# Optimization experiments

Hardware: AMD Instinct MI355X
Metric: run time of the kernel (lower is better)

The kernel has to match this reference:

```python
import jax, jax.numpy as jnp
import numpy as np

SEQ, BATCH, HIDDEN = 4096, 16, 512

def setup_inputs() -> dict:
    key = jax.random.key(0)
    kf, kx, kh = jax.random.split(key, 3)
    f = jax.random.uniform(kf, (SEQ, BATCH, HIDDEN), dtype=jnp.float32)
    x = jax.random.normal(kx, (SEQ, BATCH, HIDDEN), dtype=jnp.float32)
    hidden_init = jax.random.normal(kh, (BATCH, HIDDEN), dtype=jnp.float32)
    return {"f": f, "x": x, "hidden_init": hidden_init}

def reference(f, x, hidden_init):
    # h_t = f_t * x_t + (1 - f_t) * h_{t-1}
    # Linear recurrence h_t = a_t * h_{t-1} + b_t with a = 1-f, b = f*x.
    # Solved with an associative scan: compose (a1,b1) then (a2,b2) ->
    # (a1*a2, a2*b1 + b2). After the scan, A_t = prod(a_1..a_t) and
    # B_t = h_t assuming h_0 = 0, so h_t = B_t + A_t * h_init.
    a = 1.0 - f                      # (S, B, H)
    b = f * x                        # (S, B, H)

    def combine(c1, c2):
        a1, b1 = c1
        a2, b2 = c2
        return (a1 * a2, a2 * b1 + b2)

    A, B = jax.lax.associative_scan(combine, (a, b), axis=0)
    return B + A * hidden_init[None, :, :]
```

## Files before the change

kernel.cpp:

```cpp
#include <hip/hip_runtime.h>


#define SQ      4096
#define NC4     2048
#define NCH     8192
#define TT      32
#define NCHUNK  (SQ / TT)
#define NBLK    256
#define SEGS    16
#define CPS     (NCHUNK / SEGS)

#define AGGA_OFF  0u
#define AGGB_OFF  4194304u
#define SEGA_OFF  8388608u
#define SEGB_OFF  8912896u
#define SEGH_OFF  9437184u
#define BAR_OFF   9961472u
#define WS_NEED   (BAR_OFF + 2048u)

typedef float floatx4 __attribute__((ext_vector_type(4)));

#define FM_B(B,F,X) \
  B.x = fmaf(F.x, X.x - B.x, B.x); B.y = fmaf(F.y, X.y - B.y, B.y); \
  B.z = fmaf(F.z, X.z - B.z, B.z); B.w = fmaf(F.w, X.w - B.w, B.w);
#define FM_A(A,F) \
  A.x = fmaf(-F.x, A.x, A.x); A.y = fmaf(-F.y, A.y, A.y); \
  A.z = fmaf(-F.z, A.z, A.z); A.w = fmaf(-F.w, A.w, A.w);

__device__ __forceinline__ void grid_barrier(unsigned* bar, int gen)
{
  __syncthreads();
  if (threadIdx.x == 0) {
    __threadfence();
    __hip_atomic_fetch_add(&bar[(gen * 8 + (blockIdx.x & 7)) * 16], 1u,
                           __ATOMIC_RELEASE, __HIP_MEMORY_SCOPE_AGENT);
    unsigned sum;
    do {
      sum = 0;
#pragma unroll
      for (int s = 0; s < 8; ++s)
        sum += __hip_atomic_load(&bar[(gen * 8 + s) * 16],
                                 __ATOMIC_RELAXED, __HIP_MEMORY_SCOPE_AGENT);
      if (sum < (unsigned)NBLK) __builtin_amdgcn_s_sleep(8);
    } while (sum < (unsigned)NBLK);
    __threadfence();
  }
  __syncthreads();
}

__global__ __launch_bounds__(512, 2)
void fm_fused(const floatx4* __restrict__ f4, const floatx4* __restrict__ x4,
              const float* __restrict__ h0, char* __restrict__ ws,
              floatx4* __restrict__ out4)
{
  floatx4*  aggA4 = (floatx4*)(ws + AGGA_OFF);
  floatx4*  aggB4 = (floatx4*)(ws + AGGB_OFF);
  float*    aggAs = (float*)(ws + AGGA_OFF);
  float*    aggBs = (float*)(ws + AGGB_OFF);
  float*    segA  = (float*)(ws + SEGA_OFF);
  float*    segB  = (float*)(ws + SEGB_OFF);
  float*    segH  = (float*)(ws + SEGH_OFF);
  unsigned* bar   = (unsigned*)(ws + BAR_OFF);

  const int bid = blockIdx.x, tid = threadIdx.x;
  const int chunk = bid >> 1;
  const int c0 = ((bid & 1) << 10) + tid;
  const int c1 = c0 + 512;
  const size_t tbase = (size_t)chunk * TT * NC4;

  {
    floatx4 A0 = {1.f,1.f,1.f,1.f}, A1 = {1.f,1.f,1.f,1.f};
    floatx4 B0 = {0.f,0.f,0.f,0.f}, B1 = {0.f,0.f,0.f,0.f};
#pragma unroll 8
    for (int t = 0; t < TT; ++t) {
      const size_t r = tbase + (size_t)t * NC4;
      const floatx4 F0 = f4[r + c0], X0 = x4[r + c0];
      const floatx4 F1 = f4[r + c1], X1 = x4[r + c1];
      FM_B(B0, F0, X0)  FM_A(A0, F0)
      FM_B(B1, F1, X1)  FM_A(A1, F1)
    }
    aggA4[(size_t)chunk * NC4 + c0] = A0;
    aggA4[(size_t)chunk * NC4 + c1] = A1;
    aggB4[(size_t)chunk * NC4 + c0] = B0;
    aggB4[(size_t)chunk * NC4 + c1] = B1;
  }
  grid_barrier(bar, 0);

  {
    const int g = bid * 512 + tid;
    const int chain = g & (NCH - 1);
    const int seg   = g >> 13;
    float a = 1.f, b = 0.f;
#pragma unroll
    for (int i = 0; i < CPS; ++i) {
      const size_t idx = (size_t)(seg * CPS + i) * NCH + chain;
      const float ac = aggAs[idx], bc = aggBs[idx];
      b = fmaf(ac, b, bc);
      a *= ac;
    }
    segA[seg * NCH + chain] = a;
    segB[seg * NCH + chain] = b;
  }
  grid_barrier(bar, 1);

  if (bid < 16) {
    const int chain = bid * 512 + tid;
    float h = h0[chain];
#pragma unroll
    for (int s = 0; s < SEGS; ++s) {
      segH[s * NCH + chain] = h;
      h = fmaf(segA[s * NCH + chain], h, segB[s * NCH + chain]);
    }
  }
  grid_barrier(bar, 2);

  {
    const int g = bid * 512 + tid;
    const int chain = g & (NCH - 1);
    const int seg   = g >> 13;
    float h = segH[seg * NCH + chain];
    float a[CPS], b[CPS];
#pragma unroll
    for (int i = 0; i < CPS; ++i) {
      const size_t idx = (size_t)(seg * CPS + i) * NCH + chain;
      a[i] = aggAs[idx];
      b[i] = aggBs[idx];
    }
#pragma unroll
    for (int i = 0; i < CPS; ++i) {
      const size_t idx = (size_t)(seg * CPS + i) * NCH + chain;
      aggBs[idx] = h;
      h = fmaf(a[i], h, b[i]);
    }
  }
  grid_barrier(bar, 3);

  {
    floatx4 H0 = aggB4[(size_t)chunk * NC4 + c0];
    floatx4 H1 = aggB4[(size_t)chunk * NC4 + c1];
#pragma unroll 8
    for (int t = 0; t < TT; ++t) {
      const size_t r = tbase + (size_t)t * NC4;
      const floatx4 F0 = f4[r + c0], X0 = x4[r + c0];
      const floatx4 F1 = f4[r + c1], X1 = x4[r + c1];
      FM_B(H0, F0, X0)
      FM_B(H1, F1, X1)
      __builtin_nontemporal_store(H0, &out4[r + c0]);
      __builtin_nontemporal_store(H1, &out4[r + c1]);
    }
  }
}

#define FTT     16
#define FNCHUNK (SQ / FTT)

__global__ __launch_bounds__(256, 4)
void fm_agg(const floatx4* __restrict__ f4, const floatx4* __restrict__ x4,
            floatx4* __restrict__ aggA, floatx4* __restrict__ aggB)
{
  const int tid   = threadIdx.x;
  const int chunk = blockIdx.x >> 3;
  const int col   = ((blockIdx.x & 7) << 8) + tid;
  const size_t base = (size_t)(chunk * FTT) * NC4 + col;

  floatx4 A = {1.f,1.f,1.f,1.f}, B = {0.f,0.f,0.f,0.f};
#pragma unroll 8
  for (int t = 0; t < FTT; ++t) {
    const floatx4 F = f4[base + (size_t)t * NC4];
    const floatx4 X = x4[base + (size_t)t * NC4];
    FM_B(B, F, X)  FM_A(A, F)
  }
  aggA[(size_t)chunk * NC4 + col] = A;
  aggB[(size_t)chunk * NC4 + col] = B;
}

__global__ __launch_bounds__(256, 4)
void fm_mid(const float* __restrict__ A, float* __restrict__ B,
            const float* __restrict__ h0)
{
  const int chain = blockIdx.x * 256 + threadIdx.x;
  float h = h0[chain];
  for (int cb = 0; cb < FNCHUNK / 16; ++cb) {
    float a[16], b[16];
#pragma unroll
    for (int i = 0; i < 16; ++i) {
      const size_t idx = (size_t)(cb * 16 + i) * NCH + chain;
      a[i] = A[idx];
      b[i] = B[idx];
    }
#pragma unroll
    for (int i = 0; i < 16; ++i) {
      const size_t idx = (size_t)(cb * 16 + i) * NCH + chain;
      B[idx] = h;
      h = fmaf(a[i], h, b[i]);
    }
  }
}

__global__ __launch_bounds__(256, 4)
void fm_apply(const floatx4* __restrict__ f4, const floatx4* __restrict__ x4,
              const floatx4* __restrict__ hprev4, floatx4* __restrict__ out4)
{
  const int tid   = threadIdx.x;
  const int chunk = (FNCHUNK - 1) - (blockIdx.x >> 3);
  const int col   = ((blockIdx.x & 7) << 8) + tid;
  const size_t base = (size_t)(chunk * FTT) * NC4 + col;

  floatx4 h = hprev4[(size_t)chunk * NC4 + col];
#pragma unroll 8
  for (int t = 0; t < FTT; ++t) {
    const floatx4 F = f4[base + (size_t)t * NC4];
    const floatx4 X = x4[base + (size_t)t * NC4];
    FM_B(h, F, X)
    __builtin_nontemporal_store(h, &out4[base + (size_t)t * NC4]);
  }
}

__global__ void fm_naive(const floatx4* __restrict__ f4, const floatx4* __restrict__ x4,
                         const floatx4* __restrict__ h04, floatx4* __restrict__ out4)
{
  const int col = blockIdx.x * blockDim.x + threadIdx.x;
  if (col >= NC4) return;
  floatx4 h = h04[col];
  for (int t = 0; t < SQ; ++t) {
    const size_t idx = (size_t)t * NC4 + col;
    const floatx4 F = f4[idx], X = x4[idx];
    FM_B(h, F, X)
    out4[idx] = h;
  }
}

extern "C" void kernel_launch(void* const* d_in, const int* in_sizes, int n_in,
                              void* d_out, int out_size, void* d_ws, size_t ws_size,
                              hipStream_t stream)
{
  const floatx4* f4  = (const floatx4*)d_in[0];
  const floatx4* x4  = (const floatx4*)d_in[1];
  const float*   h0  = (const float*)d_in[2];
  floatx4* out4 = (floatx4*)d_out;

  static int coopOK = -1;
  if (coopOK < 0) {
    int dev = 0;
    hipGetDevice(&dev);
    hipDeviceProp_t prop;
    int blocksPerCU = 0;
    if (hipGetDeviceProperties(&prop, dev) == hipSuccess &&
        prop.cooperativeLaunch &&
        hipOccupancyMaxActiveBlocksPerMultiprocessor(
            &blocksPerCU, (const void*)fm_fused, 512, 0) == hipSuccess &&
        blocksPerCU >= 1 &&
        (long long)blocksPerCU * prop.multiProcessorCount >= NBLK) {
      coopOK = 1;
    } else {
      coopOK = 0;
    }
  }

  if (ws_size >= WS_NEED && coopOK == 1) {
    char* ws = (char*)d_ws;
    hipMemsetAsync(ws + BAR_OFF, 0, 2048, stream);
    void* args[5];
    args[0] = (void*)&f4; args[1] = (void*)&x4; args[2] = (void*)&h0;
    args[3] = (void*)&ws; args[4] = (void*)&out4;
    hipError_t e = hipLaunchCooperativeKernel((const void*)fm_fused,
                                              dim3(NBLK), dim3(512),
                                              args, 0, stream);
    if (e == hipSuccess) return;
    coopOK = 0;
  }

  const size_t AGG = (size_t)FNCHUNK * NC4 * 16;
  if (ws_size >= 2 * AGG) {
    floatx4* aggA = (floatx4*)d_ws;
    floatx4* aggB = (floatx4*)((char*)d_ws + AGG);
    fm_agg<<<FNCHUNK * 8, 256, 0, stream>>>(f4, x4, aggA, aggB);
    fm_mid<<<NCH / 256, 256, 0, stream>>>((const float*)aggA,
                                          (float*)aggB, h0);
    fm_apply<<<FNCHUNK * 8, 256, 0, stream>>>(f4, x4, (const floatx4*)aggB, out4);
  } else {
    fm_naive<<<(NC4 + 255) / 256, 256, 0, stream>>>(f4, x4,
                                                    (const floatx4*)h0, out4);
  }
}
```

Baseline: 374.9 us.

## Remove serial segment-carry phase and one grid barrier; launch fused kernel normally

Drops the single-block-group phase that serially propagated segment carries, along with its grid barrier. Each thread now recomputes its own segment's starting state by folding the preceding segment aggregates from h0, which adds redundant loads and FMAs, up to 15 per thread. The host side also replaces the cooperative launch and its occupancy probe with a plain kernel launch. That launch does not guarantee all 256 blocks are co-resident for the spin-wait grid barrier.

```diff
diff --git a/kernel.cpp b/kernel.cpp
--- a/kernel.cpp
+++ b/kernel.cpp
@@ -14,8 +14,7 @@
 #define AGGB_OFF  4194304u
 #define SEGA_OFF  8388608u
 #define SEGB_OFF  8912896u
-#define SEGH_OFF  9437184u
-#define BAR_OFF   9961472u
+#define BAR_OFF   9437184u
 #define WS_NEED   (BAR_OFF + 2048u)
 
 typedef float floatx4 __attribute__((ext_vector_type(4)));
@@ -59,7 +58,6 @@
   float*    aggBs = (float*)(ws + AGGB_OFF);
   float*    segA  = (float*)(ws + SEGA_OFF);
   float*    segB  = (float*)(ws + SEGB_OFF);
-  float*    segH  = (float*)(ws + SEGH_OFF);
   unsigned* bar   = (unsigned*)(ws + BAR_OFF);
 
   const int bid = blockIdx.x, tid = threadIdx.x;
@@ -103,22 +101,15 @@
   }
   grid_barrier(bar, 1);
 
-  if (bid < 16) {
-    const int chain = bid * 512 + tid;
-    float h = h0[chain];
-#pragma unroll
-    for (int s = 0; s < SEGS; ++s) {
-      segH[s * NCH + chain] = h;
-      h = fmaf(segA[s * NCH + chain], h, segB[s * NCH + chain]);
-    }
-  }
-  grid_barrier(bar, 2);
-
   {
     const int g = bid * 512 + tid;
     const int chain = g & (NCH - 1);
     const int seg   = g >> 13;
-    float h = segH[seg * NCH + chain];
+
+    float h = h0[chain];
+    for (int s = 0; s < seg; ++s)
+      h = fmaf(segA[s * NCH + chain], h, segB[s * NCH + chain]);
+
     float a[CPS], b[CPS];
 #pragma unroll
     for (int i = 0; i < CPS; ++i) {
@@ -133,7 +124,7 @@
       h = fmaf(a[i], h, b[i]);
     }
   }
-  grid_barrier(bar, 3);
+  grid_barrier(bar, 2);
 
   {
     floatx4 H0 = aggB4[(size_t)chunk * NC4 + c0];
@@ -239,35 +230,11 @@
   const float*   h0  = (const float*)d_in[2];
   floatx4* out4 = (floatx4*)d_out;
 
-  static int coopOK = -1;
-  if (coopOK < 0) {
-    int dev = 0;
-    hipGetDevice(&dev);
-    hipDeviceProp_t prop;
-    int blocksPerCU = 0;
-    if (hipGetDeviceProperties(&prop, dev) == hipSuccess &&
-        prop.cooperativeLaunch &&
-        hipOccupancyMaxActiveBlocksPerMultiprocessor(
-            &blocksPerCU, (const void*)fm_fused, 512, 0) == hipSuccess &&
-        blocksPerCU >= 1 &&
-        (long long)blocksPerCU * prop.multiProcessorCount >= NBLK) {
-      coopOK = 1;
-    } else {
-      coopOK = 0;
-    }
-  }
-
-  if (ws_size >= WS_NEED && coopOK == 1) {
+  if (ws_size >= WS_NEED) {
     char* ws = (char*)d_ws;
     hipMemsetAsync(ws + BAR_OFF, 0, 2048, stream);
-    void* args[5];
-    args[0] = (void*)&f4; args[1] = (void*)&x4; args[2] = (void*)&h0;
-    args[3] = (void*)&ws; args[4] = (void*)&out4;
-    hipError_t e = hipLaunchCooperativeKernel((const void*)fm_fused,
-                                              dim3(NBLK), dim3(512),
-                                              args, 0, stream);
-    if (e == hipSuccess) return;
-    coopOK = 0;
+    fm_fused<<<NBLK, 512, 0, stream>>>(f4, x4, h0, ws, out4);
+    return;
   }
 
   const size_t AGG = (size_t)FNCHUNK * NC4 * 16;
```

Result: slower. 436.6 us (+16.5%).
